# Optimization experiments

Hardware: AMD Instinct MI355X
Metric: run time of the kernel (lower is better)

The kernel has to match this reference:

```python
import jax, jax.numpy as jnp
import numpy as np

K = 128
HEADS = 8
B = 4
T = 2048


def setup_inputs() -> dict:
    key = jax.random.key(0)
    ks = jax.random.split(key, 6)
    x = jax.random.normal(ks[0], (B, T, K), dtype=jnp.float32)
    s = 1.0 / np.sqrt(K)
    # torch nn.Linear weights are (out_features, in_features)
    Wq = jax.random.uniform(ks[1], (HEADS * K, K), dtype=jnp.float32, minval=-s, maxval=s)
    Wk = jax.random.uniform(ks[2], (HEADS * K, K), dtype=jnp.float32, minval=-s, maxval=s)
    Wv = jax.random.uniform(ks[3], (HEADS * K, K), dtype=jnp.float32, minval=-s, maxval=s)
    su = 1.0 / np.sqrt(HEADS * K)
    Wu = jax.random.uniform(ks[4], (K, HEADS * K), dtype=jnp.float32, minval=-su, maxval=su)
    bu = jax.random.uniform(ks[5], (K,), dtype=jnp.float32, minval=-su, maxval=su)
    return {"x": x, "Wq": Wq, "Wk": Wk, "Wv": Wv, "Wu": Wu, "bu": bu}


def reference(x, Wq, Wk, Wv, Wu, bu):
    b, t, k = x.shape
    h = HEADS
    # project: Linear(k, k*h) then view(b,t,h,k); weight reshaped to (h, k_out, k_in)
    q = jnp.einsum('btk,hdk->bhtd', x, Wq.reshape(h, k, k))
    kk = jnp.einsum('btk,hdk->bhtd', x, Wk.reshape(h, k, k))
    v = jnp.einsum('btk,hdk->bhtd', x, Wv.reshape(h, k, k))
    scale = jnp.asarray(k, x.dtype) ** 0.25
    q = q / scale
    kk = kk / scale
    dot = jnp.einsum('bhtd,bhsd->bhts', q, kk)  # [b,h,t,t]
    att = jax.nn.softmax(dot, axis=-1)
    out = jnp.einsum('bhts,bhsd->bhtd', att, v)  # [b,h,t,k]
    out = out.transpose(0, 2, 1, 3).reshape(b, t, h * k)
    return out @ Wu.T + bu
```

## Files before the change

### kernel.cpp

```cpp
#include <hip/hip_runtime.h>
#include <cmath>

namespace {

constexpr int HEADS = 8;
constexpr int Bn = 4;
constexpr int Tn = 2048;
constexpr int Dn = 128;
constexpr float Q_PRESCALE = 0.1275174340f;

typedef _Float16 half8 __attribute__((ext_vector_type(8)));
typedef _Float16 half4 __attribute__((ext_vector_type(4)));
typedef _Float16 half2v __attribute__((ext_vector_type(2)));
typedef float f32x4 __attribute__((ext_vector_type(4)));
typedef float f32x16 __attribute__((ext_vector_type(16)));
typedef unsigned int u32;
typedef unsigned int u32x4 __attribute__((ext_vector_type(4)));

__global__ __launch_bounds__(256) void cast_kernel(
    const float* __restrict__ x, const float* __restrict__ Wq, const float* __restrict__ Wk,
    const float* __restrict__ Wv, const float* __restrict__ Wu, _Float16* __restrict__ xh,
    _Float16* __restrict__ WH) {
  const int idx = blockIdx.x * 256 + threadIdx.x;
  const size_t base = (size_t)idx * 8;
  const float* src;
  _Float16* dst;
  if (base < 1048576) {
    src = x + base;
    dst = xh + base;
  } else {
    const size_t r = base - 1048576;
    const int s = (int)(r >> 17);
    src = ((s == 0) ? Wq : (s == 1) ? Wk : (s == 2) ? Wv : Wu) + (r & 131071);
    dst = WH + r;
  }
  const float4 a = *reinterpret_cast<const float4*>(src);
  const float4 b = *reinterpret_cast<const float4*>(src + 4);
  half8 h;
  h[0] = (_Float16)a.x; h[1] = (_Float16)a.y; h[2] = (_Float16)a.z; h[3] = (_Float16)a.w;
  h[4] = (_Float16)b.x; h[5] = (_Float16)b.y; h[6] = (_Float16)b.z; h[7] = (_Float16)b.w;
  *reinterpret_cast<half8*>(dst) = h;
}

__global__ __launch_bounds__(256, 4) void proj_kernel(const _Float16* __restrict__ xh,
                                                      const _Float16* __restrict__ WH,
                                                      _Float16* __restrict__ Qh,
                                                      _Float16* __restrict__ Kh,
                                                      _Float16* __restrict__ Vt) {
  __shared__ _Float16 sB[128 * 136];
  const int tid = threadIdx.x;
  const int w = tid >> 6, lane = tid & 63, quad = lane >> 4, l16 = lane & 15;
  const int m0 = blockIdx.x * 128;
  const int n0 = blockIdx.y * 128;

#pragma unroll
  for (int it = 0; it < 8; ++it) {
    const int fid = tid + it * 256;
    const int r = fid >> 4, g = fid & 15;
    const half8 v = *reinterpret_cast<const half8*>(WH + (size_t)(n0 + r) * 128 + g * 8);
    const int p = g ^ (r & 15);
    *reinterpret_cast<half8*>(sB + r * 128 + p * 8) = v;
  }

  half8 af[2][4];
  const _Float16* xp = xh + (size_t)(m0 + w * 32 + l16) * 128 + quad * 8;
#pragma unroll
  for (int mt = 0; mt < 2; ++mt)
#pragma unroll
    for (int kk = 0; kk < 4; ++kk)
      af[mt][kk] = *reinterpret_cast<const half8*>(xp + mt * 16 * 128 + kk * 32);

  __syncthreads();

  f32x4 acc[2][8];
#pragma unroll
  for (int mt = 0; mt < 2; ++mt)
#pragma unroll
    for (int nt = 0; nt < 8; ++nt) acc[mt][nt] = (f32x4){0.f, 0.f, 0.f, 0.f};

#pragma unroll
  for (int kk = 0; kk < 4; ++kk)
#pragma unroll
    for (int nt = 0; nt < 8; ++nt) {
      const int r = nt * 16 + l16;
      const int p = (kk * 4 + quad) ^ l16;
      const half8 bf = *reinterpret_cast<const half8*>(sB + r * 128 + p * 8);
      acc[0][nt] = __builtin_amdgcn_mfma_f32_16x16x32_f16(af[0][kk], bf, acc[0][nt], 0, 0, 0);
      acc[1][nt] = __builtin_amdgcn_mfma_f32_16x16x32_f16(af[1][kk], bf, acc[1][nt], 0, 0, 0);
    }

  const int sel = n0 >> 10;
  const int h = (n0 >> 7) & 7;
  const int b = m0 >> 11;
  const int t0b = m0 & 2047;
  const int bh = b * HEADS + h;
  const float scale = (sel == 0) ? Q_PRESCALE : 1.0f;

  __syncthreads();

  if (sel < 2) {
#pragma unroll
    for (int mt = 0; mt < 2; ++mt)
#pragma unroll
      for (int nt = 0; nt < 8; ++nt)
#pragma unroll
        for (int r = 0; r < 4; ++r)
          sB[(w * 32 + mt * 16 + quad * 4 + r) * 136 + nt * 16 + l16] =
              (_Float16)(acc[mt][nt][r] * scale);
  } else {
#pragma unroll
    for (int mt = 0; mt < 2; ++mt)
#pragma unroll
      for (int nt = 0; nt < 8; ++nt)
#pragma unroll
        for (int r = 0; r < 4; ++r)
          sB[(nt * 16 + l16) * 136 + w * 32 + mt * 16 + quad * 4 + r] = (_Float16)acc[mt][nt][r];
  }
  __syncthreads();

  _Float16* dstbase;
  size_t rstride;
  if (sel == 0) {
    dstbase = Qh + ((size_t)bh * Tn + t0b) * Dn;
    rstride = Dn;
  } else if (sel == 1) {
    dstbase = Kh + ((size_t)bh * Tn + t0b) * Dn;
    rstride = Dn;
  } else {
    dstbase = Vt + ((size_t)bh * Dn) * Tn + t0b;
    rstride = Tn;
  }
#pragma unroll
  for (int it = 0; it < 8; ++it) {
    const int fid = tid + it * 256;
    const int r = fid >> 4, g = fid & 15;
    const half8 v = *reinterpret_cast<const half8*>(sB + r * 136 + g * 8);
    *reinterpret_cast<half8*>(dstbase + (size_t)r * rstride + g * 8) = v;
  }
}

__global__ __launch_bounds__(256, 1) void flash_kernel(const _Float16* __restrict__ Qh,
                                                       const _Float16* __restrict__ Kh,
                                                       const _Float16* __restrict__ Vt,
                                                       _Float16* __restrict__ Obh) {
  __shared__ _Float16 sAll[32768];

  const int tid = threadIdx.x;
  const int w = tid >> 6;
  const int lane = tid & 63;
  const int l31 = lane & 31;
  const int h = lane >> 5;
  const int qt = blockIdx.x;
  const int bh = blockIdx.y;
  constexpr int NT = Tn / 64;

  half8 qf[2][8];
#pragma unroll
  for (int qb = 0; qb < 2; ++qb) {
    const _Float16* Qp =
        Qh + ((size_t)bh * Tn + qt * 256 + w * 64 + qb * 32 + l31) * Dn + h * 8;
#pragma unroll
    for (int ds = 0; ds < 8; ++ds) qf[qb][ds] = *reinterpret_cast<const half8*>(Qp + ds * 16);
  }

  const _Float16* Kp = Kh + (size_t)bh * Tn * Dn;
  const _Float16* Vp = Vt + (size_t)bh * Dn * Tn;

  f32x16 o[4][2];
#pragma unroll
  for (int db = 0; db < 4; ++db)
#pragma unroll
    for (int qb = 0; qb < 2; ++qb) o[db][qb] = (f32x16)(0.f);
  float lsum[2] = {0.f, 0.f};

  half8 kreg[4], vreg[4];
  const int kr = tid >> 4, kg = tid & 15;
  const int vr = tid >> 3, vg = tid & 7;
  const int vG = (vg >> 1) * 2;
  const int vO = (vg & 1) * 4;

#pragma unroll
  for (int it = 0; it < 4; ++it) {
    kreg[it] = *reinterpret_cast<const half8*>(Kp + (size_t)(kr + it * 16) * Dn + kg * 8);
    vreg[it] = *reinterpret_cast<const half8*>(Vp + (size_t)(vr + it * 32) * Tn + vg * 8);
  }
  {
    _Float16* sK0 = sAll;
    _Float16* sV0 = sAll + 16384;
#pragma unroll
    for (int it = 0; it < 4; ++it) {
      const int r = kr + it * 16;
      const int p = kg ^ (r & 15);
      *reinterpret_cast<half8*>(sK0 + r * 128 + p * 8) = kreg[it];
      const int rv = vr + it * 32;
      const int sw = (rv & 7) ^ ((rv >> 1) & 4);
      const half8 v = vreg[it];
      half4 lo, hi;
      lo[0] = v[0]; lo[1] = v[1]; lo[2] = v[2]; lo[3] = v[3];
      hi[0] = v[4]; hi[1] = v[5]; hi[2] = v[6]; hi[3] = v[7];
      *reinterpret_cast<half4*>(sV0 + rv * 64 + ((vG ^ sw) * 8) + vO) = lo;
      *reinterpret_cast<half4*>(sV0 + rv * 64 + (((vG + 1) ^ sw) * 8) + vO) = hi;
    }
  }
#pragma unroll
  for (int it = 0; it < 4; ++it) {
    kreg[it] = *reinterpret_cast<const half8*>(Kp + (size_t)(64 + kr + it * 16) * Dn + kg * 8);
    vreg[it] = *reinterpret_cast<const half8*>(Vp + (size_t)(vr + it * 32) * Tn + 64 + vg * 8);
  }
  __syncthreads();

  f32x16 sacc[2][2];
#pragma unroll
  for (int qb = 0; qb < 2; ++qb)
#pragma unroll
    for (int kb = 0; kb < 2; ++kb) sacc[qb][kb] = (f32x16)(0.f);
#pragma unroll
  for (int ds = 0; ds < 8; ++ds) {
    half8 kf[2];
#pragma unroll
    for (int kb = 0; kb < 2; ++kb) {
      const int r = kb * 32 + l31;
      const int p = (ds * 2 + h) ^ (r & 15);
      kf[kb] = *reinterpret_cast<const half8*>(sAll + r * 128 + p * 8);
    }
#pragma unroll
    for (int qb = 0; qb < 2; ++qb)
#pragma unroll
      for (int kb = 0; kb < 2; ++kb)
        sacc[qb][kb] =
            __builtin_amdgcn_mfma_f32_32x32x16_f16(kf[kb], qf[qb][ds], sacc[qb][kb], 0, 0, 0);
  }

  for (int st = 0; st < NT; ++st) {
    const int cur = st & 1, nxt = cur ^ 1;
    _Float16* sKn = sAll + nxt * 8192;
    _Float16* sVn = sAll + 16384 + nxt * 8192;
    _Float16* sVc = sAll + 16384 + cur * 8192;

    if (st + 1 < NT) {
#pragma unroll
      for (int it = 0; it < 4; ++it) {
        const int r = kr + it * 16;
        const int p = kg ^ (r & 15);
        *reinterpret_cast<half8*>(sKn + r * 128 + p * 8) = kreg[it];
        const int rv = vr + it * 32;
        const int sw = (rv & 7) ^ ((rv >> 1) & 4);
        const half8 v = vreg[it];
        half4 lo, hi;
        lo[0] = v[0]; lo[1] = v[1]; lo[2] = v[2]; lo[3] = v[3];
        hi[0] = v[4]; hi[1] = v[5]; hi[2] = v[6]; hi[3] = v[7];
        *reinterpret_cast<half4*>(sVn + rv * 64 + ((vG ^ sw) * 8) + vO) = lo;
        *reinterpret_cast<half4*>(sVn + rv * 64 + (((vG + 1) ^ sw) * 8) + vO) = hi;
      }
    }
    if (st + 2 < NT) {
      const _Float16* knext = Kp + (size_t)(st + 2) * 64 * Dn;
      const _Float16* vnext = Vp + (st + 2) * 64;
#pragma unroll
      for (int it = 0; it < 4; ++it) {
        kreg[it] = *reinterpret_cast<const half8*>(knext + (size_t)(kr + it * 16) * Dn + kg * 8);
        vreg[it] = *reinterpret_cast<const half8*>(vnext + (size_t)(vr + it * 32) * Tn + vg * 8);
      }
    }

    half8 bfr[2][4];
#pragma unroll
    for (int qb = 0; qb < 2; ++qb) {
#pragma unroll
      for (int kb = 0; kb < 2; ++kb) {
        u32 pk[8];
        float part = 0.f;
#pragma unroll
        for (int j = 0; j < 8; ++j) {
          const float e0 = __builtin_amdgcn_exp2f(sacc[qb][kb][2 * j]);
          const float e1 = __builtin_amdgcn_exp2f(sacc[qb][kb][2 * j + 1]);
          part += e0 + e1;
          half2v hp = {(_Float16)e0, (_Float16)e1};
          pk[j] = __builtin_bit_cast(u32, hp);
        }
        lsum[qb] += part;
        u32x4 beven = {pk[0], pk[1], pk[2], pk[3]};
        u32x4 bodd = {pk[4], pk[5], pk[6], pk[7]};
        bfr[qb][kb * 2] = __builtin_bit_cast(half8, beven);
        bfr[qb][kb * 2 + 1] = __builtin_bit_cast(half8, bodd);
      }
    }

#pragma unroll
    for (int kb16 = 0; kb16 < 4; ++kb16) {
#pragma unroll
      for (int db = 0; db < 4; ++db) {
        const int r = db * 32 + l31;
        const int pv = (kb16 * 2 + h) ^ ((r & 7) ^ ((r >> 1) & 4));
        const half8 vf = *reinterpret_cast<const half8*>(sVc + r * 64 + pv * 8);
        o[db][0] = __builtin_amdgcn_mfma_f32_32x32x16_f16(vf, bfr[0][kb16], o[db][0], 0, 0, 0);
        o[db][1] = __builtin_amdgcn_mfma_f32_32x32x16_f16(vf, bfr[1][kb16], o[db][1], 0, 0, 0);
      }
    }

    __syncthreads();

    if (st + 1 < NT) {
#pragma unroll
      for (int qb = 0; qb < 2; ++qb)
#pragma unroll
        for (int kb = 0; kb < 2; ++kb) sacc[qb][kb] = (f32x16)(0.f);
#pragma unroll
      for (int ds = 0; ds < 8; ++ds) {
        half8 kf[2];
#pragma unroll
        for (int kb = 0; kb < 2; ++kb) {
          const int r = kb * 32 + l31;
          const int p = (ds * 2 + h) ^ (r & 15);
          kf[kb] = *reinterpret_cast<const half8*>(sKn + r * 128 + p * 8);
        }
#pragma unroll
        for (int qb = 0; qb < 2; ++qb)
#pragma unroll
          for (int kb = 0; kb < 2; ++kb)
            sacc[qb][kb] =
                __builtin_amdgcn_mfma_f32_32x32x16_f16(kf[kb], qf[qb][ds], sacc[qb][kb], 0, 0, 0);
      }
    }
  }

  float inv[2];
#pragma unroll
  for (int qb = 0; qb < 2; ++qb) {
    float ls = lsum[qb];
    ls += __shfl_xor(ls, 32);
    inv[qb] = 1.0f / ls;
  }

  __syncthreads();
  _Float16* const sO = sAll + w * 8192;

#pragma unroll
  for (int qb = 0; qb < 2; ++qb) {
    const int qrow = qb * 32 + l31;
#pragma unroll
    for (int db = 0; db < 4; ++db)
#pragma unroll
      for (int grp = 0; grp < 4; ++grp) {
        const int d0 = db * 32 + grp * 8 + h * 4;
        half4 hv;
#pragma unroll
        for (int i = 0; i < 4; ++i) hv[i] = (_Float16)(o[db][qb][grp * 4 + i] * inv[qb]);
        const int idx = qrow * 128 + (((d0 >> 3) ^ (qrow & 15)) << 3) + (d0 & 7);
        *reinterpret_cast<half4*>(sO + idx) = hv;
      }
  }
  const int b = bh >> 3, hh = bh & 7;
#pragma unroll
  for (int it = 0; it < 16; ++it) {
    const int idx = lane + it * 64;
    const int row = idx >> 4, g = idx & 15;
    const half8 v = *reinterpret_cast<const half8*>(sO + row * 128 + ((g ^ (row & 15)) << 3));
    const size_t t = (size_t)(b * Tn + qt * 256 + w * 64 + row);
    *reinterpret_cast<half8*>(Obh + t * (HEADS * Dn) + hh * 128 + g * 8) = v;
  }
}

__global__ __launch_bounds__(256, 2) void outproj_kernel(const _Float16* __restrict__ Obh,
                                                         const _Float16* __restrict__ Wuh,
                                                         const float* __restrict__ bu,
                                                         float* __restrict__ out) {
  __shared__ float sR[4 * 32 * 128];
  const int tid = threadIdx.x;
  const int w = tid >> 6, lane = tid & 63, quad = lane >> 4, l16 = lane & 15;
  const int r0 = blockIdx.x * 32;

  f32x4 acc[2][8];
#pragma unroll
  for (int mt = 0; mt < 2; ++mt)
#pragma unroll
    for (int nt = 0; nt < 8; ++nt) acc[mt][nt] = (f32x4){0.f, 0.f, 0.f, 0.f};

  const _Float16* ap = Obh + (size_t)(r0 + l16) * 1024 + w * 256 + quad * 8;
  const _Float16* bp = Wuh + (size_t)l16 * 1024 + w * 256 + quad * 8;

#pragma unroll
  for (int kk = 0; kk < 8; ++kk) {
    const half8 a0 = *reinterpret_cast<const half8*>(ap + kk * 32);
    const half8 a1 = *reinterpret_cast<const half8*>(ap + 16 * 1024 + kk * 32);
#pragma unroll
    for (int nt = 0; nt < 8; ++nt) {
      const half8 bf = *reinterpret_cast<const half8*>(bp + (size_t)nt * 16 * 1024 + kk * 32);
      acc[0][nt] = __builtin_amdgcn_mfma_f32_16x16x32_f16(a0, bf, acc[0][nt], 0, 0, 0);
      acc[1][nt] = __builtin_amdgcn_mfma_f32_16x16x32_f16(a1, bf, acc[1][nt], 0, 0, 0);
    }
  }

#pragma unroll
  for (int mt = 0; mt < 2; ++mt)
#pragma unroll
    for (int nt = 0; nt < 8; ++nt)
#pragma unroll
      for (int r = 0; r < 4; ++r)
        sR[w * 4096 + (mt * 16 + quad * 4 + r) * 128 + nt * 16 + l16] = acc[mt][nt][r];
  __syncthreads();

#pragma unroll
  for (int it = 0; it < 16; ++it) {
    const int idx = tid + it * 256;
    const int row = idx >> 7, col = idx & 127;
    const float v = sR[idx] + sR[4096 + idx] + sR[8192 + idx] + sR[12288 + idx] + bu[col];
    out[(size_t)(r0 + row) * Dn + col] = v;
  }
}

}

extern "C" void kernel_launch(void* const* d_in, const int* in_sizes, int n_in, void* d_out,
                              int out_size, void* d_ws, size_t ws_size, hipStream_t stream) {
  (void)in_sizes; (void)n_in; (void)out_size; (void)ws_size;
  const float* x = (const float*)d_in[0];
  const float* Wq = (const float*)d_in[1];
  const float* Wk = (const float*)d_in[2];
  const float* Wv = (const float*)d_in[3];
  const float* Wu = (const float*)d_in[4];
  const float* bu = (const float*)d_in[5];
  float* out = (float*)d_out;

  constexpr size_t NE = (size_t)Bn * HEADS * Tn * Dn;
  char* ws = (char*)d_ws;
  _Float16* xh = (_Float16*)ws;
  _Float16* WH = (_Float16*)(ws + 2097152);
  _Float16* Qh = (_Float16*)(ws + 4194304);
  _Float16* Kh = (_Float16*)(ws + 4194304 + NE * 2);
  _Float16* Vt = (_Float16*)(ws + 4194304 + NE * 4);
  _Float16* Obh = (_Float16*)(ws + 4194304 + NE * 6);
  _Float16* Wuh = WH + 393216;

  cast_kernel<<<dim3(768), 256, 0, stream>>>(x, Wq, Wk, Wv, Wu, xh, WH);
  proj_kernel<<<dim3(64, 24), 256, 0, stream>>>(xh, WH, Qh, Kh, Vt);
  flash_kernel<<<dim3(8, 32), 256, 0, stream>>>(Qh, Kh, Vt, Obh);
  outproj_kernel<<<dim3(256), 256, 0, stream>>>(Obh, Wuh, bu, out);
}
```

Before: 172.7 us.

## Software-pipeline QK^T of next tile with softmax and PV of current tile

Restructures the flash attention main loop so the S=QK^T MFMAs for the next K tile are interleaved with the exp/pack and PV MFMAs of the current tile, using ping-pong score accumulators and a triple-buffered V region in LDS. The single barrier moves to right after the LDS stores, so the next tile's QK^T can run alongside the current PV. This aims to hide exp/VALU latency behind matrix work and shorten the per-tile critical path. The cost is more live registers (two sets of score accumulators), which risks spills or lower occupancy, plus more LDS.

```diff
diff --git a/kernel.cpp b/kernel.cpp
--- a/kernel.cpp
+++ b/kernel.cpp
@@ -143,7 +143,7 @@
                                                        const _Float16* __restrict__ Kh,
                                                        const _Float16* __restrict__ Vt,
                                                        _Float16* __restrict__ Obh) {
-  __shared__ _Float16 sAll[32768];
+  __shared__ _Float16 sAll[40960];
 
   const int tid = threadIdx.x;
   const int w = tid >> 6;
@@ -209,35 +209,28 @@
   }
   __syncthreads();
 
-  f32x16 sacc[2][2];
-#pragma unroll
-  for (int qb = 0; qb < 2; ++qb)
-#pragma unroll
-    for (int kb = 0; kb < 2; ++kb) sacc[qb][kb] = (f32x16)(0.f);
+  f32x16 scA[2][2], scB[2][2];
+#pragma unroll
+  for (int a = 0; a < 2; ++a)
+#pragma unroll
+    for (int b2 = 0; b2 < 2; ++b2) scA[a][b2] = (f32x16)(0.f);
 #pragma unroll
   for (int ds = 0; ds < 8; ++ds) {
-    half8 kf[2];
-#pragma unroll
-    for (int kb = 0; kb < 2; ++kb) {
-      const int r = kb * 32 + l31;
-      const int p = (ds * 2 + h) ^ (r & 15);
-      kf[kb] = *reinterpret_cast<const half8*>(sAll + r * 128 + p * 8);
-    }
-#pragma unroll
-    for (int qb = 0; qb < 2; ++qb)
-#pragma unroll
-      for (int kb = 0; kb < 2; ++kb)
-        sacc[qb][kb] =
-            __builtin_amdgcn_mfma_f32_32x32x16_f16(kf[kb], qf[qb][ds], sacc[qb][kb], 0, 0, 0);
-  }
-
-  for (int st = 0; st < NT; ++st) {
-    const int cur = st & 1, nxt = cur ^ 1;
-    _Float16* sKn = sAll + nxt * 8192;
-    _Float16* sVn = sAll + 16384 + nxt * 8192;
-    _Float16* sVc = sAll + 16384 + cur * 8192;
-
-    if (st + 1 < NT) {
+    const int p = (ds * 2 + h) ^ (l31 & 15);
+    const half8 kf0 = *reinterpret_cast<const half8*>(sAll + l31 * 128 + p * 8);
+    const half8 kf1 = *reinterpret_cast<const half8*>(sAll + (32 + l31) * 128 + p * 8);
+    scA[0][0] = __builtin_amdgcn_mfma_f32_32x32x16_f16(kf0, qf[0][ds], scA[0][0], 0, 0, 0);
+    scA[0][1] = __builtin_amdgcn_mfma_f32_32x32x16_f16(kf1, qf[0][ds], scA[0][1], 0, 0, 0);
+    scA[1][0] = __builtin_amdgcn_mfma_f32_32x32x16_f16(kf0, qf[1][ds], scA[1][0], 0, 0, 0);
+    scA[1][1] = __builtin_amdgcn_mfma_f32_32x32x16_f16(kf1, qf[1][ds], scA[1][1], 0, 0, 0);
+  }
+
+  auto step = [&](int t, f32x16 (&sc)[2][2], f32x16 (&sn)[2][2]) {
+    _Float16* sKn = sAll + ((t + 1) & 1) * 8192;
+    _Float16* sVc = sAll + 16384 + (t % 3) * 8192;
+    _Float16* sVn = sAll + 16384 + ((t + 1) % 3) * 8192;
+
+    if (t + 1 < NT) {
 #pragma unroll
       for (int it = 0; it < 4; ++it) {
         const int r = kr + it * 16;
@@ -253,9 +246,10 @@
         *reinterpret_cast<half4*>(sVn + rv * 64 + (((vG + 1) ^ sw) * 8) + vO) = hi;
       }
     }
-    if (st + 2 < NT) {
-      const _Float16* knext = Kp + (size_t)(st + 2) * 64 * Dn;
-      const _Float16* vnext = Vp + (st + 2) * 64;
+    __syncthreads();
+    if (t + 2 < NT) {
+      const _Float16* knext = Kp + (size_t)(t + 2) * 64 * Dn;
+      const _Float16* vnext = Vp + (t + 2) * 64;
 #pragma unroll
       for (int it = 0; it < 4; ++it) {
         kreg[it] = *reinterpret_cast<const half8*>(knext + (size_t)(kr + it * 16) * Dn + kg * 8);
@@ -263,17 +257,24 @@
       }
     }
 
+    if (t + 1 < NT) {
+#pragma unroll
+      for (int a = 0; a < 2; ++a)
+#pragma unroll
+        for (int b2 = 0; b2 < 2; ++b2) sn[a][b2] = (f32x16)(0.f);
+    }
+
     half8 bfr[2][4];
 #pragma unroll
-    for (int qb = 0; qb < 2; ++qb) {
-#pragma unroll
-      for (int kb = 0; kb < 2; ++kb) {
+    for (int i = 0; i < 4; ++i) {
+      const int qb = i & 1, kb = i >> 1;
+      {
         u32 pk[8];
         float part = 0.f;
 #pragma unroll
         for (int j = 0; j < 8; ++j) {
-          const float e0 = __builtin_amdgcn_exp2f(sacc[qb][kb][2 * j]);
-          const float e1 = __builtin_amdgcn_exp2f(sacc[qb][kb][2 * j + 1]);
+          const float e0 = __builtin_amdgcn_exp2f(sc[qb][kb][2 * j]);
+          const float e1 = __builtin_amdgcn_exp2f(sc[qb][kb][2 * j + 1]);
           part += e0 + e1;
           half2v hp = {(_Float16)e0, (_Float16)e1};
           pk[j] = __builtin_bit_cast(u32, hp);
@@ -284,10 +285,33 @@
         bfr[qb][kb * 2] = __builtin_bit_cast(half8, beven);
         bfr[qb][kb * 2 + 1] = __builtin_bit_cast(half8, bodd);
       }
-    }
-
-#pragma unroll
-    for (int kb16 = 0; kb16 < 4; ++kb16) {
+      if (t + 1 < NT) {
+#pragma unroll
+        for (int dd = 0; dd < 2; ++dd) {
+          const int ds = 2 * i + dd;
+          const int p = (ds * 2 + h) ^ (l31 & 15);
+          const half8 kf0 = *reinterpret_cast<const half8*>(sKn + l31 * 128 + p * 8);
+          const half8 kf1 = *reinterpret_cast<const half8*>(sKn + (32 + l31) * 128 + p * 8);
+          sn[0][0] = __builtin_amdgcn_mfma_f32_32x32x16_f16(kf0, qf[0][ds], sn[0][0], 0, 0, 0);
+          sn[0][1] = __builtin_amdgcn_mfma_f32_32x32x16_f16(kf1, qf[0][ds], sn[0][1], 0, 0, 0);
+          sn[1][0] = __builtin_amdgcn_mfma_f32_32x32x16_f16(kf0, qf[1][ds], sn[1][0], 0, 0, 0);
+          sn[1][1] = __builtin_amdgcn_mfma_f32_32x32x16_f16(kf1, qf[1][ds], sn[1][1], 0, 0, 0);
+        }
+      }
+      if (i >= 1) {
+        const int kb16 = i - 1;
+#pragma unroll
+        for (int db = 0; db < 4; ++db) {
+          const int r = db * 32 + l31;
+          const int pv = (kb16 * 2 + h) ^ ((r & 7) ^ ((r >> 1) & 4));
+          const half8 vf = *reinterpret_cast<const half8*>(sVc + r * 64 + pv * 8);
+          o[db][0] = __builtin_amdgcn_mfma_f32_32x32x16_f16(vf, bfr[0][kb16], o[db][0], 0, 0, 0);
+          o[db][1] = __builtin_amdgcn_mfma_f32_32x32x16_f16(vf, bfr[1][kb16], o[db][1], 0, 0, 0);
+        }
+      }
+    }
+    {
+      const int kb16 = 3;
 #pragma unroll
       for (int db = 0; db < 4; ++db) {
         const int r = db * 32 + l31;
@@ -297,31 +321,11 @@
         o[db][1] = __builtin_amdgcn_mfma_f32_32x32x16_f16(vf, bfr[1][kb16], o[db][1], 0, 0, 0);
       }
     }
-
-    __syncthreads();
-
-    if (st + 1 < NT) {
-#pragma unroll
-      for (int qb = 0; qb < 2; ++qb)
-#pragma unroll
-        for (int kb = 0; kb < 2; ++kb) sacc[qb][kb] = (f32x16)(0.f);
-#pragma unroll
-      for (int ds = 0; ds < 8; ++ds) {
-        half8 kf[2];
-#pragma unroll
-        for (int kb = 0; kb < 2; ++kb) {
-          const int r = kb * 32 + l31;
-          const int p = (ds * 2 + h) ^ (r & 15);
-          kf[kb] = *reinterpret_cast<const half8*>(sKn + r * 128 + p * 8);
-        }
-#pragma unroll
-        for (int qb = 0; qb < 2; ++qb)
-#pragma unroll
-          for (int kb = 0; kb < 2; ++kb)
-            sacc[qb][kb] =
-                __builtin_amdgcn_mfma_f32_32x32x16_f16(kf[kb], qf[qb][ds], sacc[qb][kb], 0, 0, 0);
-      }
-    }
+  };
+
+  for (int st = 0; st < NT; st += 2) {
+    step(st, scA, scB);
+    step(st + 1, scB, scA);
   }
 
   float inv[2];
```

New measurement: 167.9 us. 1.03x faster.
